# Performance work log

Hardware: AMD Instinct MI355X
Metric: run time of the kernel (lower is better)

## Reference

```python
import jax, jax.numpy as jnp
import numpy as np

EPS = 1e-6
K = 20                 # k-NN neighbors (init default)
NEG_SLOPE_CONV = 0.2   # VNLinearLeakyReLU negative_slope in conv_pos / actvn_c
NEG_SLOPE_BLOCK = 0.0  # VNResnetBlockFC uses VNLeakyReLU(negative_slope=0.0)


def vn_linear(w, x):
    # w: [O, C], x: [B, C, 3, ...] -> [B, O, 3, ...]
    return jnp.einsum('oc,bc...->bo...', w, x)


def vn_leaky(x, d, slope):
    # Vector-neuron leaky ReLU: project onto learned direction d per channel.
    dot = jnp.sum(x * d, axis=2, keepdims=True)          # sum over 3-vector dim
    dsq = jnp.sum(d * d, axis=2, keepdims=True)
    x_neg = x - (dot / (dsq + EPS)) * d
    return slope * x + (1.0 - slope) * jnp.where(dot >= 0, x, x_neg)


def vn_lin_leaky(wf, wd, x, slope):
    return vn_leaky(vn_linear(wf, x), vn_linear(wd, x), slope)


def knn_idx(pts, k):
    # pts: [B, N, 3]; largest of negative squared distance = nearest (incl. self)
    d2 = jnp.sum(pts * pts, axis=-1)
    score = 2.0 * jnp.einsum('bnd,bmd->bnm', pts, pts) - d2[:, :, None] - d2[:, None, :]
    _, idx = jax.lax.top_k(score, k)
    return idx                                           # [B, N, k]


def graph_feature_cross(p, k):
    # p: [B, N, 3] -> edge features [B, 3(ch: rel, center, cross), 3(vec), N, k]
    idx = knn_idx(p, k)
    nb = jax.vmap(lambda pts, ix: pts[ix])(p, idx)       # [B, N, k, 3] gather
    ctr = jnp.broadcast_to(p[:, :, None, :], nb.shape)
    cross = jnp.cross(nb, ctr)
    feat = jnp.stack([nb - ctr, ctr, cross], axis=3)     # [B, N, k, 3ch, 3vec]
    return jnp.transpose(feat, (0, 3, 4, 1, 2))


def vn_resnet_block(x, wd0, wf0, wd1, wf1, wsc):
    net = vn_linear(wf0, vn_leaky(x, vn_linear(wd0, x), NEG_SLOPE_BLOCK))
    dx = vn_linear(wf1, vn_leaky(net, vn_linear(wd1, net), NEG_SLOPE_BLOCK))
    return vn_linear(wsc, x) + dx


def setup_inputs() -> dict:
    key = jax.random.key(0)
    ks = jax.random.split(key, 11)
    B, N = 4, 2048
    c_dim, hd = 128, 128
    s = lambda k_, sh, fan: (jax.random.normal(k_, sh, jnp.float32) / np.sqrt(fan).astype(np.float32))
    return {
        'p': jax.random.normal(ks[0], (B, N, 3), jnp.float32),
        'w_conv_feat': s(ks[1], (128, 3), 3),
        'w_conv_dir': s(ks[2], (128, 3), 3),
        'w_fc_pos': s(ks[3], (2 * hd, 128), 128),
        'blk_dir0': s(ks[4], (5, 2 * hd, 2 * hd), 2 * hd),
        'blk_fc0': s(ks[5], (5, hd, 2 * hd), 2 * hd),
        'blk_dir1': s(ks[6], (5, hd, hd), hd),
        'blk_fc1': s(ks[7], (5, hd, hd), hd),
        'blk_sc': s(ks[8], (5, hd, 2 * hd), 2 * hd),
        'w_actc_dir': s(ks[9], (hd, hd), hd),
        'w_fc_c': s(ks[10], (c_dim, hd), hd),
    }


def reference(p, w_conv_feat, w_conv_dir, w_fc_pos, blk_dir0, blk_fc0,
              blk_dir1, blk_fc1, blk_sc, w_actc_dir, w_fc_c):
    feat = graph_feature_cross(p, K)                     # [B, 3, 3, N, K]
    net = vn_lin_leaky(w_conv_feat, w_conv_dir, feat, NEG_SLOPE_CONV)
    net = net.mean(axis=-1)                              # pool over k -> [B,128,3,N]
    net = vn_linear(w_fc_pos, net)                       # [B,256,3,N]
    net = vn_resnet_block(net, blk_dir0[0], blk_fc0[0], blk_dir1[0], blk_fc1[0], blk_sc[0])
    for i in range(1, 5):                                # fixed 5-block stack
        pooled = jnp.broadcast_to(net.mean(axis=-1, keepdims=True), net.shape)
        net = jnp.concatenate([net, pooled], axis=1)     # [B,256,3,N]
        net = vn_resnet_block(net, blk_dir0[i], blk_fc0[i], blk_dir1[i], blk_fc1[i], blk_sc[i])
    net = net.mean(axis=-1)                              # global pool -> [B,128,3]
    net = vn_leaky(net, vn_linear(w_actc_dir, net), NEG_SLOPE_CONV)
    return vn_linear(w_fc_c, net)                        # c: [B,128,3]
```

## Files before the change

### kernel.cpp

```cpp
#include <hip/hip_runtime.h>
#include <math.h>

#define NPT 2048
#define BB 4
#define KNN 20
#define EPSV 1e-6f

typedef unsigned short u16;
typedef unsigned int u32;
typedef _Float16 half8 __attribute__((ext_vector_type(8)));
typedef __attribute__((ext_vector_type(4))) float f32x4;
typedef __attribute__((ext_vector_type(4))) u32 uint4v;

#define MFMAH(a,b,c) __builtin_amdgcn_mfma_f32_16x16x32_f16((a),(b),(c),0,0,0)

__device__ __forceinline__ u16 f2h(float f) {
    _Float16 h = (_Float16)f;
    return __builtin_bit_cast(u16, h);
}
__device__ __forceinline__ float h2f(u16 b) {
    return (float)__builtin_bit_cast(_Float16, b);
}

__global__ __launch_bounds__(256)
void knn_edge_kernel(const float* __restrict__ p,
                     const float* __restrict__ wf, const float* __restrict__ wd,
                     u16* __restrict__ net1) {
    int bn = blockIdx.x;
    int b = bn >> 11, n = bn & (NPT - 1);
    const float* pb = p + (size_t)b * NPT * 3;
    float qx = pb[n*3+0], qy = pb[n*3+1], qz = pb[n*3+2];
    float qq = qx*qx + qy*qy + qz*qz;
    __shared__ u32 keys[NPT];
    __shared__ int hist[4][256];
    __shared__ int wtot[4];
    __shared__ int sh_byte, sh_ngt, sure_cnt, tie_cnt;
    __shared__ int tie_m[64];
    __shared__ int sel[KNN];
    __shared__ float nb[KNN][3];
    int tid = threadIdx.x;
    int lane = tid & 63, wv = tid >> 6;
    for (int m = tid; m < NPT; m += 256) {
        float px = pb[m*3+0], py = pb[m*3+1], pz = pb[m*3+2];
        float sc = 2.f*(qx*px + qy*py + qz*pz) - qq - (px*px + py*py + pz*pz);
        u32 u = __builtin_bit_cast(u32, sc);
        keys[m] = u ^ (u32)(((int)u >> 31) | (int)0x80000000);
    }
    if (tid == 0) { sure_cnt = 0; tie_cnt = 0; }
    __syncthreads();
    u32 prefix = 0; int need = KNN;
    for (int pass = 3; pass >= 0; --pass) {
        int shift = pass * 8;
        u32 maskhi = (pass == 3) ? 0u : (0xFFFFFFFFu << (shift + 8));
        hist[0][tid] = 0; hist[1][tid] = 0; hist[2][tid] = 0; hist[3][tid] = 0;
        __syncthreads();
        int prevbin = -1, cnt = 0;
        #pragma unroll
        for (int j = 0; j < 8; ++j) {
            u32 key = keys[tid + 256*j];
            int bin = ((key & maskhi) == (prefix & maskhi)) ? (int)((key >> shift) & 255) : -1;
            if (bin == prevbin) { ++cnt; }
            else {
                if (prevbin >= 0) atomicAdd(&hist[wv][prevbin], cnt);
                prevbin = bin; cnt = 1;
            }
        }
        if (prevbin >= 0) atomicAdd(&hist[wv][prevbin], cnt);
        __syncthreads();
        int own = hist[0][tid] + hist[1][tid] + hist[2][tid] + hist[3][tid];
        int sum = own;
        #pragma unroll
        for (int off = 1; off < 64; off <<= 1) {
            int v = __shfl_down(sum, off, 64);
            if (lane + off < 64) sum += v;
        }
        if (lane == 0) wtot[wv] = sum;
        __syncthreads();
        int addhi = 0;
        #pragma unroll
        for (int w2 = 0; w2 < 4; ++w2) if (w2 > wv) addhi += wtot[w2];
        int cnt_ge = sum + addhi;
        int cnt_gt = cnt_ge - own;
        if (cnt_ge >= need && cnt_gt < need) { sh_byte = tid; sh_ngt = cnt_gt; }
        __syncthreads();
        prefix |= ((u32)sh_byte) << shift;
        need -= sh_ngt;
        __syncthreads();
    }
    u32 T = prefix;
    #pragma unroll
    for (int j = 0; j < 8; ++j) {
        int m = tid + 256*j;
        u32 key = keys[m];
        if (key > T) {
            int slot = atomicAdd(&sure_cnt, 1);
            sel[slot] = m;
        } else if (key == T) {
            int t = atomicAdd(&tie_cnt, 1);
            if (t < 64) tie_m[t] = m;
        }
    }
    __syncthreads();
    if (tid == 0) {
        int base = sure_cnt;
        int r = KNN - base;
        int tc = tie_cnt;
        if (tc == r) {
            for (int t2 = 0; t2 < r; ++t2) sel[base + t2] = tie_m[t2];
        } else if (tc <= 64) {
            for (int t2 = 0; t2 < r; ++t2) {
                int best = 1 << 30, bj = 0;
                for (int t3 = 0; t3 < tc; ++t3)
                    if (tie_m[t3] < best) { best = tie_m[t3]; bj = t3; }
                tie_m[bj] = 1 << 30;
                sel[base + t2] = best;
            }
        } else {
            int got = 0;
            for (int m = 0; m < NPT && got < r; ++m)
                if (keys[m] == T) { sel[base + got] = m; ++got; }
        }
    }
    __syncthreads();
    if (tid < KNN) {
        int j = sel[tid];
        nb[tid][0] = pb[j*3+0]; nb[tid][1] = pb[j*3+1]; nb[tid][2] = pb[j*3+2];
    }
    __syncthreads();
    {
        float* part = (float*)keys;
        int o = tid & 127, kh = tid >> 7;
        float wfa = wf[o*3+0], wfb = wf[o*3+1], wfc = wf[o*3+2];
        float wda = wd[o*3+0], wdb = wd[o*3+1], wdc = wd[o*3+2];
        float cx = qx, cy = qy, cz = qz;
        float a0 = 0.f, a1 = 0.f, a2 = 0.f;
        int k0 = kh * 10;
        #pragma unroll
        for (int k = 0; k < 10; ++k) {
            float nx = nb[k0+k][0], ny = nb[k0+k][1], nz = nb[k0+k][2];
            float rx = nx-cx, ry = ny-cy, rz = nz-cz;
            float sx = ny*cz - nz*cy;
            float sy = nz*cx - nx*cz;
            float sz = nx*cy - ny*cx;
            float fx = wfa*rx + wfb*cx + wfc*sx;
            float fy = wfa*ry + wfb*cy + wfc*sy;
            float fz = wfa*rz + wfb*cz + wfc*sz;
            float dx0 = wda*rx + wdb*cx + wdc*sx;
            float dy0 = wda*ry + wdb*cy + wdc*sy;
            float dz0 = wda*rz + wdb*cz + wdc*sz;
            float dot = fx*dx0 + fy*dy0 + fz*dz0;
            float dsq = dx0*dx0 + dy0*dy0 + dz0*dz0;
            float t = dot / (dsq + EPSV);
            bool pos = dot >= 0.f;
            float gx = pos ? fx : (fx - t*dx0);
            float gy = pos ? fy : (fy - t*dy0);
            float gz = pos ? fz : (fz - t*dz0);
            a0 += 0.2f*fx + 0.8f*gx;
            a1 += 0.2f*fy + 0.8f*gy;
            a2 += 0.2f*fz + 0.8f*gz;
        }
        if (kh == 1) { part[o*3+0] = a0; part[o*3+1] = a1; part[o*3+2] = a2; }
        __syncthreads();
        if (kh == 0) {
            a0 += part[o*3+0]; a1 += part[o*3+1]; a2 += part[o*3+2];
            const float s = 1.f / (float)KNN;
            net1[(size_t)(b*6144 +          n)*128 + o] = f2h(a0*s);
            net1[(size_t)(b*6144 + 2048  + n)*128 + o] = f2h(a1*s);
            net1[(size_t)(b*6144 + 4096  + n)*128 + o] = f2h(a2*s);
        }
    }
}

template<int O, int C1, int C2, bool POOL, bool BIASED>
__global__ __launch_bounds__(256) void gemm_plain(
    const u16* __restrict__ W1, int ldw1,
    const u16* __restrict__ X1, int sx1,
    const u16* __restrict__ W2, int ldw2,
    const u16* __restrict__ X2, int sx2,
    const float* __restrict__ WscF, const float* __restrict__ PmPrev,
    u16* __restrict__ Y, int sy,
    float* __restrict__ PmOut)
{
    __shared__ __align__(16) char smem[64*132*4];
    __shared__ float pms[128];
    __shared__ float biasS_s[128];
    const int m0 = blockIdx.x * 64;
    const int ob = blockIdx.y * 128;
    const int b   = m0 / 6144;
    const int vec = (m0 % 6144) / 2048;
    const int tid = threadIdx.x;
    const int lane = tid & 63;
    const int wid = __builtin_amdgcn_readfirstlane(tid >> 6);
    const int wr = wid & 1, wc = wid >> 1;
    const int l15 = lane & 15, l4 = lane >> 4;

    if (BIASED) {
        if (tid < 128) pms[tid] = PmPrev[(size_t)(b*128 + tid)*3 + vec];
        __syncthreads();
        if (tid < 128) {
            const float* wrow = WscF + (size_t)tid*256 + 128;
            float s = 0.f;
            #pragma unroll 4
            for (int c = 0; c < 128; ++c) s += wrow[c]*pms[c];
            biasS_s[tid] = s;
        }
        __syncthreads();
    }

    f32x4 acc[4][2];
    #pragma unroll
    for (int io = 0; io < 4; ++io) {
        float bv[4];
        #pragma unroll
        for (int r = 0; r < 4; ++r)
            bv[r] = BIASED ? biasS_s[wr*64 + io*16 + l4*4 + r] : 0.f;
        #pragma unroll
        for (int jc = 0; jc < 2; ++jc)
            #pragma unroll
            for (int r = 0; r < 4; ++r) acc[io][jc][r] = bv[r];
    }

    constexpr int NS = (C1 + C2) / 64;
    auto ldaddr = [&](int st, int u) -> const u16* {
        const bool ph2 = (st >= C1/64);
        const u16* w = ph2 ? W2 : W1; const u16* x = ph2 ? X2 : X1;
        int ldw = ph2 ? ldw2 : ldw1; int sx = ph2 ? sx2 : sx1;
        int cc = (ph2 ? (st - C1/64) : st) * 64;
        if (u < 1024) {
            int row = u >> 3, q = u & 7;
            return w + (size_t)(ob + row)*ldw + cc + q*8;
        }
        int uu = u - 1024;
        int row = uu >> 3, q = uu & 7;
        return x + (size_t)(m0 + row)*sx + cc + q*8;
    };
    auto lds_dst = [&](int u) -> char* {
        if (u < 1024) { int row = u >> 3, q = u & 7; return smem + row*144 + q*16; }
        int uu = u - 1024;
        int row = uu >> 3, q = uu & 7;
        return smem + 18432 + row*144 + q*16;
    };

    uint4v pf[6];
    #pragma unroll
    for (int j = 0; j < 6; ++j) pf[j] = *reinterpret_cast<const uint4v*>(ldaddr(0, tid + 256*j));
    #pragma unroll
    for (int j = 0; j < 6; ++j) *reinterpret_cast<uint4v*>(lds_dst(tid + 256*j)) = pf[j];

    for (int st = 0; st < NS; ++st) {
        __syncthreads();
        if (st + 1 < NS) {
            #pragma unroll
            for (int j = 0; j < 6; ++j)
                pf[j] = *reinterpret_cast<const uint4v*>(ldaddr(st+1, tid + 256*j));
        }
        #pragma unroll
        for (int ks = 0; ks < 2; ++ks) {
            half8 fA[4], fB[2];
            #pragma unroll
            for (int io = 0; io < 4; ++io)
                fA[io] = *reinterpret_cast<const half8*>(smem + (wr*64 + io*16 + l15)*144 + ks*64 + l4*16);
            #pragma unroll
            for (int i = 0; i < 2; ++i)
                fB[i] = *reinterpret_cast<const half8*>(smem + 18432 + (wc*32 + i*16 + l15)*144 + ks*64 + l4*16);
            #pragma unroll
            for (int io = 0; io < 4; ++io)
                #pragma unroll
                for (int jc = 0; jc < 2; ++jc)
                    acc[io][jc] = MFMAH(fA[io], fB[jc], acc[io][jc]);
        }
        __syncthreads();
        if (st + 1 < NS) {
            #pragma unroll
            for (int j = 0; j < 6; ++j)
                *reinterpret_cast<uint4v*>(lds_dst(tid + 256*j)) = pf[j];
        }
    }

    float* sd = (float*)smem;
    #pragma unroll
    for (int io = 0; io < 4; ++io)
        #pragma unroll
        for (int jc = 0; jc < 2; ++jc) {
            int jj = wc*32 + jc*16 + l15;
            int orow = wr*64 + io*16 + l4*4;
            *reinterpret_cast<f32x4*>(sd + jj*132 + orow) = acc[io][jc];
        }
    __syncthreads();

    #pragma unroll
    for (int rep = 0; rep < 4; ++rep) {
        int task = tid + 256*rep;
        int oc = task & 15, ml = task >> 4;
        const float* dp = sd + ml*132 + oc*8;
        u32 hw[4];
        #pragma unroll
        for (int e2 = 0; e2 < 4; ++e2)
            hw[e2] = (u32)f2h(dp[2*e2]) | ((u32)f2h(dp[2*e2+1]) << 16);
        *reinterpret_cast<uint4v*>(Y + (size_t)(m0 + ml)*sy + ob + oc*8) =
            (uint4v){hw[0],hw[1],hw[2],hw[3]};
    }

    if (POOL) {
        int o_l = tid & 127, half = tid >> 7;
        float sum = 0.f;
        #pragma unroll 8
        for (int c = 0; c < 32; ++c) sum += sd[(half*32 + c)*132 + o_l];
        atomicAdd(&PmOut[(size_t)(b*128 + o_l)*3 + vec], sum * (1.f/(float)NPT));
    }
}

template<int O, int CIN, bool VIRT>
__global__ __launch_bounds__(256) void gemm_dir(
    const u16* __restrict__ W_, int ldw,
    const u16* __restrict__ X1, int sx,
    const float* __restrict__ WdF, const float* __restrict__ Pm,
    u16* __restrict__ Ov, int so,
    float* __restrict__ PmZero)
{
    __shared__ __align__(16) char smem[96*132*4];
    __shared__ float pmd[384];
    __shared__ float biasD_s[384];
    const int gx = blockIdx.x;
    const int b  = gx >> 6;
    const int n0 = (gx & 63) * 32;
    const int ob = blockIdx.y * 128;
    const int tid = threadIdx.x;
    const int lane = tid & 63;
    const int wid = __builtin_amdgcn_readfirstlane(tid >> 6);
    const int wr = wid & 1, wc = wid >> 1;
    const int l15 = lane & 15, l4 = lane >> 4;

    if (PmZero != nullptr && gx == 0 && blockIdx.y == 0)
        for (int t = tid; t < 1536; t += 256) PmZero[t] = 0.f;

    if (VIRT) {
        for (int t = tid; t < 384; t += 256) pmd[t] = Pm[(size_t)b*384 + t];
        __syncthreads();
        for (int t = tid; t < 384; t += 256) {
            int o_l = t / 3, v = t - o_l*3;
            const float* wrow = WdF + (size_t)(ob + o_l)*256 + 128;
            float s = 0.f;
            #pragma unroll 4
            for (int c = 0; c < 128; ++c) s += wrow[c]*pmd[c*3 + v];
            biasD_s[t] = s;
        }
        __syncthreads();
    }

    f32x4 acc[4][3];
    #pragma unroll
    for (int io = 0; io < 4; ++io)
        #pragma unroll
        for (int jc = 0; jc < 3; ++jc) {
            int v = (wc*48 + jc*16) >> 5;
            #pragma unroll
            for (int r = 0; r < 4; ++r) {
                int o_l = wr*64 + io*16 + l4*4 + r;
                acc[io][jc][r] = VIRT ? biasD_s[o_l*3 + v] : 0.f;
            }
        }

    constexpr int NS = CIN / 64;
    auto ldaddr = [&](int st, int u) -> const u16* {
        int cc = st*64;
        if (u < 1024) {
            int row = u >> 3, q = u & 7;
            return W_ + (size_t)(ob + row)*ldw + cc + q*8;
        }
        int uu = u - 1024;
        int row = uu >> 3, q = uu & 7;
        int m = b*6144 + (row >> 5)*2048 + n0 + (row & 31);
        return X1 + (size_t)m*sx + cc + q*8;
    };
    auto lds_dst = [&](int u) -> char* {
        if (u < 1024) { int row = u >> 3, q = u & 7; return smem + row*144 + q*16; }
        int uu = u - 1024;
        int row = uu >> 3, q = uu & 7;
        return smem + 18432 + row*144 + q*16;
    };

    uint4v pf[7];
    #pragma unroll
    for (int j = 0; j < 7; ++j) pf[j] = *reinterpret_cast<const uint4v*>(ldaddr(0, tid + 256*j));
    #pragma unroll
    for (int j = 0; j < 7; ++j) *reinterpret_cast<uint4v*>(lds_dst(tid + 256*j)) = pf[j];

    for (int st = 0; st < NS; ++st) {
        __syncthreads();
        if (st + 1 < NS) {
            #pragma unroll
            for (int j = 0; j < 7; ++j)
                pf[j] = *reinterpret_cast<const uint4v*>(ldaddr(st+1, tid + 256*j));
        }
        #pragma unroll
        for (int ks = 0; ks < 2; ++ks) {
            half8 fA[4], fB[3];
            #pragma unroll
            for (int io = 0; io < 4; ++io)
                fA[io] = *reinterpret_cast<const half8*>(smem + (wr*64 + io*16 + l15)*144 + ks*64 + l4*16);
            #pragma unroll
            for (int i = 0; i < 3; ++i)
                fB[i] = *reinterpret_cast<const half8*>(smem + 18432 + (wc*48 + i*16 + l15)*144 + ks*64 + l4*16);
            #pragma unroll
            for (int io = 0; io < 4; ++io)
                #pragma unroll
                for (int jc = 0; jc < 3; ++jc)
                    acc[io][jc] = MFMAH(fA[io], fB[jc], acc[io][jc]);
        }
        __syncthreads();
        if (st + 1 < NS) {
            #pragma unroll
            for (int j = 0; j < 7; ++j)
                *reinterpret_cast<uint4v*>(lds_dst(tid + 256*j)) = pf[j];
        }
    }

    float* sd = (float*)smem;
    #pragma unroll
    for (int io = 0; io < 4; ++io)
        #pragma unroll
        for (int jc = 0; jc < 3; ++jc) {
            int jj = wc*48 + jc*16 + l15;
            int orow = wr*64 + io*16 + l4*4;
            *reinterpret_cast<f32x4*>(sd + jj*132 + orow) = acc[io][jc];
        }
    __syncthreads();

    #pragma unroll
    for (int rep = 0; rep < 2; ++rep) {
        int task = tid + 256*rep;
        int oc = task & 15, nl = (task >> 4) & 31;
        float d[3][8], x[3][8];
        #pragma unroll
        for (int v = 0; v < 3; ++v) {
            const float* dp = sd + (v*32 + nl)*132 + oc*8;
            #pragma unroll
            for (int e = 0; e < 8; ++e) d[v][e] = dp[e];
        }
        if (VIRT && ob != 0) {
            #pragma unroll
            for (int e = 0; e < 8; ++e) {
                int c = oc*8 + e;
                #pragma unroll
                for (int v = 0; v < 3; ++v)
                    x[v][e] = Pm[(size_t)(b*128 + c)*3 + v];
            }
        } else {
            #pragma unroll
            for (int v = 0; v < 3; ++v) {
                size_t m = (size_t)(b*6144 + v*2048 + n0 + nl);
                uint4v hx = *reinterpret_cast<const uint4v*>(X1 + m*sx + ob + oc*8);
                #pragma unroll
                for (int w = 0; w < 4; ++w) {
                    x[v][2*w]   = h2f((u16)(hx[w] & 0xffffu));
                    x[v][2*w+1] = h2f((u16)(hx[w] >> 16));
                }
            }
        }
        #pragma unroll
        for (int e = 0; e < 8; ++e) {
            float d0 = d[0][e], d1 = d[1][e], d2 = d[2][e];
            float dot = x[0][e]*d0 + x[1][e]*d1 + x[2][e]*d2;
            float dsq = d0*d0 + d1*d1 + d2*d2;
            float t = dot / (dsq + EPSV);
            if (dot < 0.f) { x[0][e] -= t*d0; x[1][e] -= t*d1; x[2][e] -= t*d2; }
        }
        #pragma unroll
        for (int v = 0; v < 3; ++v) {
            u32 hw[4];
            #pragma unroll
            for (int e2 = 0; e2 < 4; ++e2)
                hw[e2] = (u32)f2h(x[v][2*e2]) | ((u32)f2h(x[v][2*e2+1]) << 16);
            *reinterpret_cast<uint4v*>(Ov + (size_t)(b*6144 + v*2048 + n0 + nl)*so + ob + oc*8) =
                (uint4v){hw[0],hw[1],hw[2],hw[3]};
        }
    }
}

template<int CSC, bool VIRT>
__global__ __launch_bounds__(256) void fused_back(
    const u16* __restrict__ Wd,
    const u16* __restrict__ Wf1,
    const u16* __restrict__ Wsc,
    const float* __restrict__ WsF,
    const u16* __restrict__ T_,
    const u16* __restrict__ Xs,
    const float* __restrict__ Pm,
    u16* __restrict__ Y,
    float* __restrict__ PmOut)
{
    __shared__ __align__(16) char smem[76800];
    __shared__ float pms[384];
    __shared__ float biasS_s[384];
    constexpr int U_OFF = 0;
    constexpr int W_OFF = 26112;
    constexpr int X_OFF = 44544;
    const int gx = blockIdx.x;
    const int b  = gx >> 6;
    const int n0 = (gx & 63) * 32;
    const int tid = threadIdx.x;
    const int lane = tid & 63;
    const int wid = __builtin_amdgcn_readfirstlane(tid >> 6);
    const int wr = wid & 1, wc = wid >> 1;
    const int l15 = lane & 15, l4 = lane >> 4;

    if (VIRT) {
        for (int t = tid; t < 384; t += 256) pms[t] = Pm[(size_t)b*384 + t];
        __syncthreads();
        for (int t = tid; t < 384; t += 256) {
            int o_l = t / 3, v = t - o_l*3;
            const float* wrow = WsF + (size_t)o_l*256 + 128;
            float s = 0.f;
            #pragma unroll 4
            for (int c = 0; c < 128; ++c) s += wrow[c]*pms[c*3 + v];
            biasS_s[t] = s;
        }
        __syncthreads();
    }

    f32x4 acc1[4][3];
    #pragma unroll
    for (int io = 0; io < 4; ++io)
        #pragma unroll
        for (int jc = 0; jc < 3; ++jc)
            acc1[io][jc] = (f32x4){0.f,0.f,0.f,0.f};

    auto ld1 = [&](int st, int u) -> const u16* {
        int cc = st*64;
        if (u < 1024) { int row = u >> 3, q = u & 7; return Wd + (size_t)row*128 + cc + q*8; }
        int uu = u - 1024;
        int row = uu >> 3, q = uu & 7;
        int m = b*6144 + (row >> 5)*2048 + n0 + (row & 31);
        return T_ + (size_t)m*128 + cc + q*8;
    };
    auto st1 = [&](int u) -> char* {
        if (u < 1024) { int row = u >> 3, q = u & 7; return smem + W_OFF + row*144 + q*16; }
        int uu = u - 1024;
        int row = uu >> 3, q = uu & 7;
        return smem + X_OFF + row*144 + q*16;
    };

    uint4v pf[7];
    #pragma unroll
    for (int j = 0; j < 7; ++j) pf[j] = *reinterpret_cast<const uint4v*>(ld1(0, tid + 256*j));
    #pragma unroll
    for (int j = 0; j < 7; ++j) *reinterpret_cast<uint4v*>(st1(tid + 256*j)) = pf[j];

    for (int st = 0; st < 2; ++st) {
        __syncthreads();
        if (st + 1 < 2) {
            #pragma unroll
            for (int j = 0; j < 7; ++j)
                pf[j] = *reinterpret_cast<const uint4v*>(ld1(st+1, tid + 256*j));
        }
        #pragma unroll
        for (int ks = 0; ks < 2; ++ks) {
            half8 fA[4], fB[3];
            #pragma unroll
            for (int io = 0; io < 4; ++io)
                fA[io] = *reinterpret_cast<const half8*>(smem + W_OFF + (wr*64 + io*16 + l15)*144 + ks*64 + l4*16);
            #pragma unroll
            for (int i = 0; i < 3; ++i)
                fB[i] = *reinterpret_cast<const half8*>(smem + X_OFF + (wc*48 + i*16 + l15)*144 + ks*64 + l4*16);
            #pragma unroll
            for (int io = 0; io < 4; ++io)
                #pragma unroll
                for (int jc = 0; jc < 3; ++jc)
                    acc1[io][jc] = MFMAH(fA[io], fB[jc], acc1[io][jc]);
        }
        __syncthreads();
        if (st + 1 < 2) {
            #pragma unroll
            for (int j = 0; j < 7; ++j)
                *reinterpret_cast<uint4v*>(st1(tid + 256*j)) = pf[j];
        }
    }

    float* sd = (float*)(smem + W_OFF);
    #pragma unroll
    for (int io = 0; io < 4; ++io)
        #pragma unroll
        for (int jc = 0; jc < 3; ++jc) {
            int jj = wc*48 + jc*16 + l15;
            int orow = wr*64 + io*16 + l4*4;
            *reinterpret_cast<f32x4*>(sd + jj*132 + orow) = acc1[io][jc];
        }
    __syncthreads();
    #pragma unroll
    for (int rep = 0; rep < 2; ++rep) {
        int task = tid + 256*rep;
        int oc = task & 15, nl = (task >> 4) & 31;
        float d[3][8], x[3][8];
        #pragma unroll
        for (int v = 0; v < 3; ++v) {
            const float* dp = sd + (v*32 + nl)*132 + oc*8;
            #pragma unroll
            for (int e = 0; e < 8; ++e) d[v][e] = dp[e];
        }
        #pragma unroll
        for (int v = 0; v < 3; ++v) {
            size_t m = (size_t)(b*6144 + v*2048 + n0 + nl);
            uint4v hx = *reinterpret_cast<const uint4v*>(T_ + m*128 + oc*8);
            #pragma unroll
            for (int w = 0; w < 4; ++w) {
                x[v][2*w]   = h2f((u16)(hx[w] & 0xffffu));
                x[v][2*w+1] = h2f((u16)(hx[w] >> 16));
            }
        }
        #pragma unroll
        for (int e = 0; e < 8; ++e) {
            float d0 = d[0][e], d1 = d[1][e], d2 = d[2][e];
            float dot = x[0][e]*d0 + x[1][e]*d1 + x[2][e]*d2;
            float dsq = d0*d0 + d1*d1 + d2*d2;
            float t = dot / (dsq + EPSV);
            if (dot < 0.f) { x[0][e] -= t*d0; x[1][e] -= t*d1; x[2][e] -= t*d2; }
        }
        #pragma unroll
        for (int v = 0; v < 3; ++v) {
            u32 hw[4];
            #pragma unroll
            for (int e2 = 0; e2 < 4; ++e2)
                hw[e2] = (u32)f2h(x[v][2*e2]) | ((u32)f2h(x[v][2*e2+1]) << 16);
            *reinterpret_cast<uint4v*>(smem + U_OFF + (v*32 + nl)*272 + oc*16) =
                (uint4v){hw[0],hw[1],hw[2],hw[3]};
        }
    }
    __syncthreads();

    f32x4 acc2[4][3];
    #pragma unroll
    for (int io = 0; io < 4; ++io)
        #pragma unroll
        for (int jc = 0; jc < 3; ++jc) {
            int v = (wc*48 + jc*16) >> 5;
            #pragma unroll
            for (int r = 0; r < 4; ++r) {
                int o_l = wr*64 + io*16 + l4*4 + r;
                acc2[io][jc][r] = VIRT ? biasS_s[o_l*3 + v] : 0.f;
            }
        }

    constexpr int NS2 = 2 + CSC/64;
    auto ld2 = [&](int st, int u) -> const u16* {
        if (st < 2) {
            int row = u >> 3, q = u & 7;
            return Wf1 + (size_t)row*128 + st*64 + q*8;
        }
        int cc = (st - 2)*64;
        if (u < 1024) { int row = u >> 3, q = u & 7; return Wsc + (size_t)row*256 + cc + q*8; }
        int uu = u - 1024;
        int row = uu >> 3, q = uu & 7;
        int m = b*6144 + (row >> 5)*2048 + n0 + (row & 31);
        return Xs + (size_t)m*CSC + cc + q*8;
    };

    #pragma unroll
    for (int j = 0; j < 7; ++j) { int u = tid + 256*j; if (u < 1024) pf[j] = *reinterpret_cast<const uint4v*>(ld2(0, u)); }
    #pragma unroll
    for (int j = 0; j < 7; ++j) { int u = tid + 256*j; if (u < 1024) *reinterpret_cast<uint4v*>(st1(u)) = pf[j]; }

    for (int st = 0; st < NS2; ++st) {
        __syncthreads();
        int nv = (st + 1 < 2) ? 1024 : 1792;
        if (st + 1 < NS2) {
            #pragma unroll
            for (int j = 0; j < 7; ++j) { int u = tid + 256*j; if (u < nv) pf[j] = *reinterpret_cast<const uint4v*>(ld2(st+1, u)); }
        }
        #pragma unroll
        for (int ks = 0; ks < 2; ++ks) {
            half8 fA[4], fB[3];
            #pragma unroll
            for (int io = 0; io < 4; ++io)
                fA[io] = *reinterpret_cast<const half8*>(smem + W_OFF + (wr*64 + io*16 + l15)*144 + ks*64 + l4*16);
            if (st < 2) {
                #pragma unroll
                for (int i = 0; i < 3; ++i)
                    fB[i] = *reinterpret_cast<const half8*>(smem + U_OFF + (wc*48 + i*16 + l15)*272 + st*128 + ks*64 + l4*16);
            } else {
                #pragma unroll
                for (int i = 0; i < 3; ++i)
                    fB[i] = *reinterpret_cast<const half8*>(smem + X_OFF + (wc*48 + i*16 + l15)*144 + ks*64 + l4*16);
            }
            #pragma unroll
            for (int io = 0; io < 4; ++io)
                #pragma unroll
                for (int jc = 0; jc < 3; ++jc)
                    acc2[io][jc] = MFMAH(fA[io], fB[jc], acc2[io][jc]);
        }
        __syncthreads();
        if (st + 1 < NS2) {
            #pragma unroll
            for (int j = 0; j < 7; ++j) { int u = tid + 256*j; if (u < nv) *reinterpret_cast<uint4v*>(st1(u)) = pf[j]; }
        }
    }

    #pragma unroll
    for (int io = 0; io < 4; ++io)
        #pragma unroll
        for (int jc = 0; jc < 3; ++jc) {
            int jj = wc*48 + jc*16 + l15;
            int orow = wr*64 + io*16 + l4*4;
            *reinterpret_cast<f32x4*>(sd + jj*132 + orow) = acc2[io][jc];
        }
    __syncthreads();
    #pragma unroll
    for (int rep = 0; rep < 2; ++rep) {
        int task = tid + 256*rep;
        int oc = task & 15, nl = (task >> 4) & 31;
        #pragma unroll
        for (int v = 0; v < 3; ++v) {
            const float* dp = sd + (v*32 + nl)*132 + oc*8;
            u32 hw[4];
            #pragma unroll
            for (int e2 = 0; e2 < 4; ++e2)
                hw[e2] = (u32)f2h(dp[2*e2]) | ((u32)f2h(dp[2*e2+1]) << 16);
            *reinterpret_cast<uint4v*>(Y + (size_t)(b*6144 + v*2048 + n0 + nl)*128 + oc*8) =
                (uint4v){hw[0],hw[1],hw[2],hw[3]};
        }
    }
    for (int t = tid; t < 384; t += 256) {
        int v = t >> 7, o_l = t & 127;
        float sum = 0.f;
        #pragma unroll 8
        for (int nl = 0; nl < 32; ++nl) sum += sd[(v*32 + nl)*132 + o_l];
        atomicAdd(&PmOut[(size_t)(b*128 + o_l)*3 + v], sum * (1.f/(float)NPT));
    }
}

#define WO_FCPOS 0
#define WO_DIR0  32768
#define WO_FC0   360448
#define WO_DIR1  524288
#define WO_FC1   606208
#define WO_SC    688128
#define WTOT     851968
__global__ __launch_bounds__(256)
void convert_w_kernel(const float* __restrict__ s0, const float* __restrict__ s1,
                      const float* __restrict__ s2, const float* __restrict__ s3,
                      const float* __restrict__ s4, const float* __restrict__ s5,
                      u16* __restrict__ Wf) {
    int t = blockIdx.x*256 + threadIdx.x;
    if (t >= WTOT) return;
    const float* src; int base;
    if      (t < WO_DIR0) { src = s0; base = WO_FCPOS; }
    else if (t < WO_FC0)  { src = s1; base = WO_DIR0; }
    else if (t < WO_DIR1) { src = s2; base = WO_FC0; }
    else if (t < WO_FC1)  { src = s3; base = WO_DIR1; }
    else if (t < WO_SC)   { src = s4; base = WO_FC1; }
    else                  { src = s5; base = WO_SC; }
    Wf[t] = f2h(src[t - base]);
}

__global__ __launch_bounds__(128)
void final_head_kernel(const float* __restrict__ q, const float* __restrict__ Wdir,
                       const float* __restrict__ Wfc, float* __restrict__ out) {
    int b = blockIdx.x; int o = threadIdx.x;
    __shared__ float qs[128][3];
    __shared__ float zs[128][3];
    qs[o][0] = q[((size_t)b*128 + o)*3 + 0];
    qs[o][1] = q[((size_t)b*128 + o)*3 + 1];
    qs[o][2] = q[((size_t)b*128 + o)*3 + 2];
    __syncthreads();
    float d0 = 0.f, d1 = 0.f, d2 = 0.f;
    for (int c = 0; c < 128; ++c) {
        float w = Wdir[o*128 + c];
        d0 += w*qs[c][0]; d1 += w*qs[c][1]; d2 += w*qs[c][2];
    }
    float x0 = qs[o][0], x1 = qs[o][1], x2 = qs[o][2];
    float dot = d0*x0 + d1*x1 + d2*x2;
    float dsq = d0*d0 + d1*d1 + d2*d2;
    float t = dot / (dsq + EPSV);
    bool pos = dot >= 0.f;
    float g0 = pos ? x0 : (x0 - t*d0);
    float g1 = pos ? x1 : (x1 - t*d1);
    float g2 = pos ? x2 : (x2 - t*d2);
    zs[o][0] = 0.2f*x0 + 0.8f*g0;
    zs[o][1] = 0.2f*x1 + 0.8f*g1;
    zs[o][2] = 0.2f*x2 + 0.8f*g2;
    __syncthreads();
    float c0 = 0.f, c1 = 0.f, c2 = 0.f;
    for (int c = 0; c < 128; ++c) {
        float w = Wfc[o*128 + c];
        c0 += w*zs[c][0]; c1 += w*zs[c][1]; c2 += w*zs[c][2];
    }
    out[((size_t)b*128 + o)*3 + 0] = c0;
    out[((size_t)b*128 + o)*3 + 1] = c1;
    out[((size_t)b*128 + o)*3 + 2] = c2;
}

extern "C" void kernel_launch(void* const* d_in, const int* in_sizes, int n_in,
                              void* d_out, int out_size, void* d_ws, size_t ws_size,
                              hipStream_t stream) {
    const float* p           = (const float*)d_in[0];
    const float* w_conv_feat = (const float*)d_in[1];
    const float* w_conv_dir  = (const float*)d_in[2];
    const float* w_fc_pos    = (const float*)d_in[3];
    const float* blk_dir0    = (const float*)d_in[4];
    const float* blk_fc0     = (const float*)d_in[5];
    const float* blk_dir1    = (const float*)d_in[6];
    const float* blk_fc1     = (const float*)d_in[7];
    const float* blk_sc      = (const float*)d_in[8];
    const float* w_actc_dir  = (const float*)d_in[9];
    const float* w_fc_c      = (const float*)d_in[10];
    float* out = (float*)d_out;

    char* wsb = (char*)d_ws;
    size_t cur = 0;
    auto carve = [&](size_t nbytes) -> char* {
        char* r = wsb + cur;
        cur += (nbytes + 255) & ~(size_t)255;
        return r;
    };
    const size_t MTOT = (size_t)BB*3*NPT;
    float* Pm0   = (float*)carve(1536*4);
    float* Pm1   = (float*)carve(1536*4);
    u16* Wf    = (u16*)carve((size_t)WTOT*2);
    u16* net1  = (u16*)carve(MTOT*128*2);
    u16* X0    = (u16*)carve(MTOT*256*2);
    u16* Ab    = (u16*)carve(MTOT*256*2);
    u16* Yb    = (u16*)carve(MTOT*128*2);
    float* PmBuf[2] = { Pm0, Pm1 };

    convert_w_kernel<<<(WTOT+255)/256, 256, 0, stream>>>(
        w_fc_pos, blk_dir0, blk_fc0, blk_dir1, blk_fc1, blk_sc, Wf);
    knn_edge_kernel<<<BB*NPT, 256, 0, stream>>>(p, w_conv_feat, w_conv_dir, net1);

    gemm_plain<256,128,0,false,false><<<dim3(384,2), 256, 0, stream>>>(
        Wf+WO_FCPOS, 128, net1, 128,
        nullptr, 0, nullptr, 0,
        nullptr, nullptr, X0, 256, nullptr);

    const u16* Yp = nullptr;
    for (int i = 0; i < 5; ++i) {
        size_t od0 = WO_DIR0 + (size_t)i*65536;
        size_t of0 = WO_FC0  + (size_t)i*32768;
        size_t od1 = WO_DIR1 + (size_t)i*16384;
        size_t of1 = WO_FC1  + (size_t)i*16384;
        size_t osc = WO_SC   + (size_t)i*32768;
        float* PmPrev = PmBuf[(i+1) & 1];
        float* PmCur  = PmBuf[i & 1];

        if (i == 0) {
            gemm_dir<256,256,false><<<dim3(BB*64,2), 256, 0, stream>>>(
                Wf+od0, 256, X0, 256, nullptr, nullptr, Ab, 256, PmCur);
        } else {
            gemm_dir<256,128,true><<<dim3(BB*64,2), 256, 0, stream>>>(
                Wf+od0, 256, Yp, 128,
                blk_dir0 + (size_t)i*65536, PmPrev, Ab, 256, PmCur);
        }
        gemm_plain<128,256,0,false,false><<<dim3(384,1), 256, 0, stream>>>(
            Wf+of0, 256, Ab, 256,
            nullptr, 0, nullptr, 0,
            nullptr, nullptr, net1, 128, nullptr);

        u16* outv = (i % 2 == 0) ? Yb : X0;
        if (i == 0) {
            fused_back<256,false><<<BB*64, 256, 0, stream>>>(
                Wf+od1, Wf+of1, Wf+osc, nullptr,
                net1, X0, nullptr, outv, PmCur);
        } else {
            fused_back<128,true><<<BB*64, 256, 0, stream>>>(
                Wf+od1, Wf+of1, Wf+osc, blk_sc + (size_t)i*32768,
                net1, Yp, PmPrev, outv, PmCur);
        }
        Yp = outv;
    }

    final_head_kernel<<<BB, 128, 0, stream>>>(PmBuf[0], w_actc_dir, w_fc_c, out);
}
```

Baseline: 316.1 us.

## Fuse fc0 GEMM into fused_back kernel, removing the separate gemm_plain launch

The fc0 linear layer (256->128) is now computed inside fused_back from the activations buffer Ab, and its result stays in shared memory. It is then consumed directly by the dir1 GEMM and the VN-leaky step. This removes one kernel launch per residual block and the global write and re-read of the intermediate net1 tensor. In exchange, fused_back does more serial work per block with only 256 blocks and slightly more shared memory. It also carries a leftover dead loop that adds extra barriers and shared-memory reads.

```diff
diff --git a/kernel.cpp b/kernel.cpp
--- a/kernel.cpp
+++ b/kernel.cpp
@@ -480,22 +480,23 @@
 
 template<int CSC, bool VIRT>
 __global__ __launch_bounds__(256) void fused_back(
+    const u16* __restrict__ Wf0,
     const u16* __restrict__ Wd,
     const u16* __restrict__ Wf1,
     const u16* __restrict__ Wsc,
     const float* __restrict__ WsF,
-    const u16* __restrict__ T_,
+    const u16* __restrict__ A_,
     const u16* __restrict__ Xs,
     const float* __restrict__ Pm,
     u16* __restrict__ Y,
     float* __restrict__ PmOut)
 {
-    __shared__ __align__(16) char smem[76800];
+    __shared__ __align__(16) char smem[77568];
     __shared__ float pms[384];
     __shared__ float biasS_s[384];
-    constexpr int U_OFF = 0;
-    constexpr int W_OFF = 26112;
-    constexpr int X_OFF = 44544;
+    constexpr int T_OFF = 0;
+    constexpr int U_OFF = 26112;
+    constexpr int SW    = 52224;
     const int gx = blockIdx.x;
     const int b  = gx >> 6;
     const int n0 = (gx & 63) * 32;
@@ -519,114 +520,230 @@
         __syncthreads();
     }
 
-    f32x4 acc1[4][3];
+    uint4v pf[7];
+
+    {
+        f32x4 accT[4][3];
+        #pragma unroll
+        for (int io = 0; io < 4; ++io)
+            #pragma unroll
+            for (int jc = 0; jc < 3; ++jc)
+                accT[io][jc] = (f32x4){0.f,0.f,0.f,0.f};
+
+        auto ldA = [&](int st, int u) -> const u16* {
+            int cc = st*64;
+            if (u < 1024) { int row = u >> 3, q = u & 7; return Wf0 + (size_t)row*256 + cc + q*8; }
+            int uu = u - 1024;
+            int row = uu >> 3, q = uu & 7;
+            int m = b*6144 + (row >> 5)*2048 + n0 + (row & 31);
+            return A_ + (size_t)m*256 + cc + q*8;
+        };
+        auto stA = [&](int u) -> char* {
+            if (u < 1024) { int row = u >> 3, q = u & 7; return smem + SW + row*144 + q*16; }
+            int uu = u - 1024;
+            int row = uu >> 3, q = uu & 7;
+            return smem + T_OFF + row*144 + q*16;
+        };
+
+        #pragma unroll
+        for (int j = 0; j < 7; ++j) pf[j] = *reinterpret_cast<const uint4v*>(ldA(0, tid + 256*j));
+        #pragma unroll
+        for (int j = 0; j < 7; ++j) *reinterpret_cast<uint4v*>(stA(tid + 256*j)) = pf[j];
+
+        for (int st = 0; st < 4; ++st) {
+            __syncthreads();
+            if (st + 1 < 4) {
+                #pragma unroll
+                for (int j = 0; j < 7; ++j)
+                    pf[j] = *reinterpret_cast<const uint4v*>(ldA(st+1, tid + 256*j));
+            }
+            #pragma unroll
+            for (int ks = 0; ks < 2; ++ks) {
+                half8 fA[4], fB[3];
+                #pragma unroll
+                for (int io = 0; io < 4; ++io)
+                    fA[io] = *reinterpret_cast<const half8*>(smem + SW + (wr*64 + io*16 + l15)*144 + ks*64 + l4*16);
+                #pragma unroll
+                for (int i = 0; i < 3; ++i)
+                    fB[i] = *reinterpret_cast<const half8*>(smem + T_OFF + (wc*48 + i*16 + l15)*144 + ks*64 + l4*16);
+                #pragma unroll
+                for (int io = 0; io < 4; ++io)
+                    #pragma unroll
+                    for (int jc = 0; jc < 3; ++jc)
+                        accT[io][jc] = MFMAH(fA[io], fB[jc], accT[io][jc]);
+            }
+            __syncthreads();
+            if (st + 1 < 4) {
+                #pragma unroll
+                for (int j = 0; j < 7; ++j)
+                    *reinterpret_cast<uint4v*>(stA(tid + 256*j)) = pf[j];
+            }
+        }
+
+        float* sdT = (float*)(smem + U_OFF);
+        #pragma unroll
+        for (int io = 0; io < 4; ++io)
+            #pragma unroll
+            for (int jc = 0; jc < 3; ++jc) {
+                int jj = wc*48 + jc*16 + l15;
+                int orow = wr*64 + io*16 + l4*4;
+                *reinterpret_cast<f32x4*>(sdT + jj*132 + orow) = accT[io][jc];
+            }
+        __syncthreads();
+        #pragma unroll
+        for (int rep = 0; rep < 2; ++rep) {
+            int task = tid + 256*rep;
+            int oc = task & 15, col = (task >> 4) & 31, v = 0;
+            int cidx = (task >> 4);
+            (void)col; (void)v; (void)cidx;
+        }
+        #pragma unroll
+        for (int rep = 0; rep < 6; ++rep) {
+            int task = tid + 256*rep;
+            int oc = task & 15, cidx = task >> 4;
+            const float* dp = sdT + cidx*132 + oc*8;
+            u32 hw[4];
+            #pragma unroll
+            for (int e2 = 0; e2 < 4; ++e2)
+                hw[e2] = (u32)f2h(dp[2*e2]) | ((u32)f2h(dp[2*e2+1]) << 16);
+            *reinterpret_cast<uint4v*>(smem + T_OFF + cidx*272 + oc*16) =
+                (uint4v){hw[0],hw[1],hw[2],hw[3]};
+        }
+        __syncthreads();
+    }
+
+    f32x4 accD[4][3];
     #pragma unroll
     for (int io = 0; io < 4; ++io)
         #pragma unroll
         for (int jc = 0; jc < 3; ++jc)
-            acc1[io][jc] = (f32x4){0.f,0.f,0.f,0.f};
-
-    auto ld1 = [&](int st, int u) -> const u16* {
-        int cc = st*64;
-        if (u < 1024) { int row = u >> 3, q = u & 7; return Wd + (size_t)row*128 + cc + q*8; }
-        int uu = u - 1024;
-        int row = uu >> 3, q = uu & 7;
-        int m = b*6144 + (row >> 5)*2048 + n0 + (row & 31);
-        return T_ + (size_t)m*128 + cc + q*8;
-    };
-    auto st1 = [&](int u) -> char* {
-        if (u < 1024) { int row = u >> 3, q = u & 7; return smem + W_OFF + row*144 + q*16; }
-        int uu = u - 1024;
-        int row = uu >> 3, q = uu & 7;
-        return smem + X_OFF + row*144 + q*16;
-    };
-
-    uint4v pf[7];
-    #pragma unroll
-    for (int j = 0; j < 7; ++j) pf[j] = *reinterpret_cast<const uint4v*>(ld1(0, tid + 256*j));
-    #pragma unroll
-    for (int j = 0; j < 7; ++j) *reinterpret_cast<uint4v*>(st1(tid + 256*j)) = pf[j];
-
-    for (int st = 0; st < 2; ++st) {
-        __syncthreads();
-        if (st + 1 < 2) {
-            #pragma unroll
-            for (int j = 0; j < 7; ++j)
-                pf[j] = *reinterpret_cast<const uint4v*>(ld1(st+1, tid + 256*j));
-        }
-        #pragma unroll
-        for (int ks = 0; ks < 2; ++ks) {
-            half8 fA[4], fB[3];
-            #pragma unroll
-            for (int io = 0; io < 4; ++io)
-                fA[io] = *reinterpret_cast<const half8*>(smem + W_OFF + (wr*64 + io*16 + l15)*144 + ks*64 + l4*16);
-            #pragma unroll
-            for (int i = 0; i < 3; ++i)
-                fB[i] = *reinterpret_cast<const half8*>(smem + X_OFF + (wc*48 + i*16 + l15)*144 + ks*64 + l4*16);
-            #pragma unroll
-            for (int io = 0; io < 4; ++io)
-                #pragma unroll
-                for (int jc = 0; jc < 3; ++jc)
-                    acc1[io][jc] = MFMAH(fA[io], fB[jc], acc1[io][jc]);
-        }
-        __syncthreads();
-        if (st + 1 < 2) {
-            #pragma unroll
-            for (int j = 0; j < 7; ++j)
-                *reinterpret_cast<uint4v*>(st1(tid + 256*j)) = pf[j];
-        }
-    }
-
-    float* sd = (float*)(smem + W_OFF);
-    #pragma unroll
-    for (int io = 0; io < 4; ++io)
-        #pragma unroll
-        for (int jc = 0; jc < 3; ++jc) {
-            int jj = wc*48 + jc*16 + l15;
-            int orow = wr*64 + io*16 + l4*4;
-            *reinterpret_cast<f32x4*>(sd + jj*132 + orow) = acc1[io][jc];
-        }
-    __syncthreads();
-    #pragma unroll
-    for (int rep = 0; rep < 2; ++rep) {
-        int task = tid + 256*rep;
-        int oc = task & 15, nl = (task >> 4) & 31;
-        float d[3][8], x[3][8];
-        #pragma unroll
-        for (int v = 0; v < 3; ++v) {
-            const float* dp = sd + (v*32 + nl)*132 + oc*8;
-            #pragma unroll
-            for (int e = 0; e < 8; ++e) d[v][e] = dp[e];
-        }
-        #pragma unroll
-        for (int v = 0; v < 3; ++v) {
-            size_t m = (size_t)(b*6144 + v*2048 + n0 + nl);
-            uint4v hx = *reinterpret_cast<const uint4v*>(T_ + m*128 + oc*8);
-            #pragma unroll
-            for (int w = 0; w < 4; ++w) {
-                x[v][2*w]   = h2f((u16)(hx[w] & 0xffffu));
-                x[v][2*w+1] = h2f((u16)(hx[w] >> 16));
-            }
-        }
-        #pragma unroll
-        for (int e = 0; e < 8; ++e) {
-            float d0 = d[0][e], d1 = d[1][e], d2 = d[2][e];
-            float dot = x[0][e]*d0 + x[1][e]*d1 + x[2][e]*d2;
-            float dsq = d0*d0 + d1*d1 + d2*d2;
-            float t = dot / (dsq + EPSV);
-            if (dot < 0.f) { x[0][e] -= t*d0; x[1][e] -= t*d1; x[2][e] -= t*d2; }
-        }
-        #pragma unroll
-        for (int v = 0; v < 3; ++v) {
-            u32 hw[4];
-            #pragma unroll
-            for (int e2 = 0; e2 < 4; ++e2)
-                hw[e2] = (u32)f2h(x[v][2*e2]) | ((u32)f2h(x[v][2*e2+1]) << 16);
-            *reinterpret_cast<uint4v*>(smem + U_OFF + (v*32 + nl)*272 + oc*16) =
-                (uint4v){hw[0],hw[1],hw[2],hw[3]};
-        }
-    }
-    __syncthreads();
+            accD[io][jc] = (f32x4){0.f,0.f,0.f,0.f};
+    {
+        auto ldW = [&](int st, int u) -> const u16* {
+            int row = u >> 3, q = u & 7;
+            return Wd + (size_t)row*128 + st*64 + q*8;
+        };
+        #pragma unroll
+        for (int j = 0; j < 4; ++j) pf[j] = *reinterpret_cast<const uint4v*>(ldW(0, tid + 256*j));
+        #pragma unroll
+        for (int j = 0; j < 4; ++j) { int u = tid + 256*j; int row = u >> 3, q = u & 7;
+            *reinterpret_cast<uint4v*>(smem + SW + row*144 + q*16) = pf[j]; }
+
+        for (int st = 0; st < 2; ++st) {
+            __syncthreads();
+            if (st + 1 < 2) {
+                #pragma unroll
+                for (int j = 0; j < 4; ++j)
+                    pf[j] = *reinterpret_cast<const uint4v*>(ldW(st+1, tid + 256*j));
+            }
+            #pragma unroll
+            for (int ks = 0; ks < 2; ++ks) {
+                half8 fA[4], fB[3];
+                #pragma unroll
+                for (int io = 0; io < 4; ++io)
+                    fA[io] = *reinterpret_cast<const half8*>(smem + SW + (wr*64 + io*16 + l15)*144 + ks*64 + l4*16);
+                #pragma unroll
+                for (int i = 0; i < 3; ++i)
+                    fB[i] = *reinterpret_cast<const half8*>(smem + T_OFF + (wc*48 + i*16 + l15)*272 + st*128 + ks*64 + l4*16);
+                #pragma unroll
+                for (int io = 0; io < 4; ++io)
+                    #pragma unroll
+                    for (int jc = 0; jc < 3; ++jc)
+                        accD[io][jc] = MFMAH(fA[io], fB[jc], accD[io][jc]);
+            }
+            __syncthreads();
+            if (st + 1 < 2) {
+                #pragma unroll
+                for (int j = 0; j < 4; ++j) { int u = tid + 256*j; int row = u >> 3, q = u & 7;
+                    *reinterpret_cast<uint4v*>(smem + SW + row*144 + q*16) = pf[j]; }
+            }
+        }
+    }
+
+    {
+        float* sdh = (float*)(smem + SW);
+        #pragma unroll
+        for (int h = 0; h < 2; ++h) {
+            if (wc == h) {
+                #pragma unroll
+                for (int io = 0; io < 4; ++io)
+                    #pragma unroll
+                    for (int jc = 0; jc < 3; ++jc) {
+                        int jl = jc*16 + l15;
+                        int orow = wr*64 + io*16 + l4*4;
+                        *reinterpret_cast<f32x4*>(sdh + jl*132 + orow) = accD[io][jc];
+                    }
+            }
+            __syncthreads();
+            #pragma unroll
+            for (int rep = 0; rep < 3; ++rep) {
+                int task = tid + 256*rep;
+                int oc = task & 15, cl = task >> 4;
+                int col = h*48 + cl;
+                const float* dp = sdh + cl*132 + oc*8;
+                float d[8], x[8];
+                #pragma unroll
+                for (int e = 0; e < 8; ++e) d[e] = dp[e];
+                uint4v hx = *reinterpret_cast<const uint4v*>(smem + T_OFF + col*272 + oc*16);
+                #pragma unroll
+                for (int w = 0; w < 4; ++w) {
+                    x[2*w]   = h2f((u16)(hx[w] & 0xffffu));
+                    x[2*w+1] = h2f((u16)(hx[w] >> 16));
+                }
+                (void)d; (void)x; (void)col;
+            }
+            __syncthreads();
+        }
+    }
+    {
+        float* sdT = (float*)(smem + U_OFF);
+        __syncthreads();
+        #pragma unroll
+        for (int io = 0; io < 4; ++io)
+            #pragma unroll
+            for (int jc = 0; jc < 3; ++jc) {
+                int jj = wc*48 + jc*16 + l15;
+                int orow = wr*64 + io*16 + l4*4;
+                *reinterpret_cast<f32x4*>(sdT + jj*132 + orow) = accD[io][jc];
+            }
+        __syncthreads();
+        #pragma unroll
+        for (int rep = 0; rep < 2; ++rep) {
+            int task = tid + 256*rep;
+            int oc = task & 15, nl = task >> 4;
+            float d[3][8], x[3][8];
+            #pragma unroll
+            for (int v = 0; v < 3; ++v) {
+                const float* dp = sdT + (v*32 + nl)*132 + oc*8;
+                #pragma unroll
+                for (int e = 0; e < 8; ++e) d[v][e] = dp[e];
+                uint4v hx = *reinterpret_cast<const uint4v*>(smem + T_OFF + (v*32 + nl)*272 + oc*16);
+                #pragma unroll
+                for (int w = 0; w < 4; ++w) {
+                    x[v][2*w]   = h2f((u16)(hx[w] & 0xffffu));
+                    x[v][2*w+1] = h2f((u16)(hx[w] >> 16));
+                }
+            }
+            #pragma unroll
+            for (int e = 0; e < 8; ++e) {
+                float d0 = d[0][e], d1 = d[1][e], d2 = d[2][e];
+                float dot = x[0][e]*d0 + x[1][e]*d1 + x[2][e]*d2;
+                float dsq = d0*d0 + d1*d1 + d2*d2;
+                float t = dot / (dsq + EPSV);
+                if (dot < 0.f) { x[0][e] -= t*d0; x[1][e] -= t*d1; x[2][e] -= t*d2; }
+            }
+            #pragma unroll
+            for (int v = 0; v < 3; ++v) {
+                u32 hw[4];
+                #pragma unroll
+                for (int e2 = 0; e2 < 4; ++e2)
+                    hw[e2] = (u32)f2h(x[v][2*e2]) | ((u32)f2h(x[v][2*e2+1]) << 16);
+                *reinterpret_cast<uint4v*>(smem + T_OFF + (v*32 + nl)*272 + oc*16) =
+                    (uint4v){hw[0],hw[1],hw[2],hw[3]};
+            }
+        }
+        __syncthreads();
+    }
 
     f32x4 acc2[4][3];
     #pragma unroll
@@ -654,11 +771,17 @@
         int m = b*6144 + (row >> 5)*2048 + n0 + (row & 31);
         return Xs + (size_t)m*CSC + cc + q*8;
     };
+    auto st2 = [&](int u) -> char* {
+        if (u < 1024) { int row = u >> 3, q = u & 7; return smem + SW + row*144 + q*16; }
+        int uu = u - 1024;
+        int row = uu >> 3, q = uu & 7;
+        return smem + U_OFF + row*144 + q*16;
+    };
 
     #pragma unroll
     for (int j = 0; j < 7; ++j) { int u = tid + 256*j; if (u < 1024) pf[j] = *reinterpret_cast<const uint4v*>(ld2(0, u)); }
     #pragma unroll
-    for (int j = 0; j < 7; ++j) { int u = tid + 256*j; if (u < 1024) *reinterpret_cast<uint4v*>(st1(u)) = pf[j]; }
+    for (int j = 0; j < 7; ++j) { int u = tid + 256*j; if (u < 1024) *reinterpret_cast<uint4v*>(st2(u)) = pf[j]; }
 
     for (int st = 0; st < NS2; ++st) {
         __syncthreads();
@@ -672,15 +795,15 @@
             half8 fA[4], fB[3];
             #pragma unroll
             for (int io = 0; io < 4; ++io)
-                fA[io] = *reinterpret_cast<const half8*>(smem + W_OFF + (wr*64 + io*16 + l15)*144 + ks*64 + l4*16);
+                fA[io] = *reinterpret_cast<const half8*>(smem + SW + (wr*64 + io*16 + l15)*144 + ks*64 + l4*16);
             if (st < 2) {
                 #pragma unroll
                 for (int i = 0; i < 3; ++i)
-                    fB[i] = *reinterpret_cast<const half8*>(smem + U_OFF + (wc*48 + i*16 + l15)*272 + st*128 + ks*64 + l4*16);
+                    fB[i] = *reinterpret_cast<const half8*>(smem + T_OFF + (wc*48 + i*16 + l15)*272 + st*128 + ks*64 + l4*16);
             } else {
                 #pragma unroll
                 for (int i = 0; i < 3; ++i)
-                    fB[i] = *reinterpret_cast<const half8*>(smem + X_OFF + (wc*48 + i*16 + l15)*144 + ks*64 + l4*16);
+                    fB[i] = *reinterpret_cast<const half8*>(smem + U_OFF + (wc*48 + i*16 + l15)*144 + ks*64 + l4*16);
             }
             #pragma unroll
             for (int io = 0; io < 4; ++io)
@@ -691,17 +814,18 @@
         __syncthreads();
         if (st + 1 < NS2) {
             #pragma unroll
-            for (int j = 0; j < 7; ++j) { int u = tid + 256*j; if (u < nv) *reinterpret_cast<uint4v*>(st1(u)) = pf[j]; }
-        }
-    }
-
+            for (int j = 0; j < 7; ++j) { int u = tid + 256*j; if (u < nv) *reinterpret_cast<uint4v*>(st2(u)) = pf[j]; }
+        }
+    }
+
+    float* sdE = (float*)smem;
     #pragma unroll
     for (int io = 0; io < 4; ++io)
         #pragma unroll
         for (int jc = 0; jc < 3; ++jc) {
             int jj = wc*48 + jc*16 + l15;
             int orow = wr*64 + io*16 + l4*4;
-            *reinterpret_cast<f32x4*>(sd + jj*132 + orow) = acc2[io][jc];
+            *reinterpret_cast<f32x4*>(sdE + jj*132 + orow) = acc2[io][jc];
         }
     __syncthreads();
     #pragma unroll
@@ -710,7 +834,7 @@
         int oc = task & 15, nl = (task >> 4) & 31;
         #pragma unroll
         for (int v = 0; v < 3; ++v) {
-            const float* dp = sd + (v*32 + nl)*132 + oc*8;
+            const float* dp = sdE + (v*32 + nl)*132 + oc*8;
             u32 hw[4];
             #pragma unroll
             for (int e2 = 0; e2 < 4; ++e2)
@@ -723,7 +847,7 @@
         int v = t >> 7, o_l = t & 127;
         float sum = 0.f;
         #pragma unroll 8
-        for (int nl = 0; nl < 32; ++nl) sum += sd[(v*32 + nl)*132 + o_l];
+        for (int nl = 0; nl < 32; ++nl) sum += sdE[(v*32 + nl)*132 + o_l];
         atomicAdd(&PmOut[(size_t)(b*128 + o_l)*3 + v], sum * (1.f/(float)NPT));
     }
 }
@@ -849,20 +973,16 @@
                 Wf+od0, 256, Yp, 128,
                 blk_dir0 + (size_t)i*65536, PmPrev, Ab, 256, PmCur);
         }
-        gemm_plain<128,256,0,false,false><<<dim3(384,1), 256, 0, stream>>>(
-            Wf+of0, 256, Ab, 256,
-            nullptr, 0, nullptr, 0,
-            nullptr, nullptr, net1, 128, nullptr);
 
         u16* outv = (i % 2 == 0) ? Yb : X0;
         if (i == 0) {
             fused_back<256,false><<<BB*64, 256, 0, stream>>>(
-                Wf+od1, Wf+of1, Wf+osc, nullptr,
-                net1, X0, nullptr, outv, PmCur);
+                Wf+of0, Wf+od1, Wf+of1, Wf+osc, nullptr,
+                Ab, X0, nullptr, outv, PmCur);
         } else {
             fused_back<128,true><<<BB*64, 256, 0, stream>>>(
-                Wf+od1, Wf+of1, Wf+osc, blk_sc + (size_t)i*32768,
-                net1, Yp, PmPrev, outv, PmCur);
+                Wf+of0, Wf+od1, Wf+of1, Wf+osc, blk_sc + (size_t)i*32768,
+                Ab, Yp, PmPrev, outv, PmCur);
         }
         Yp = outv;
     }
```

Result: faster. 291.3 us (-7.8%).
